# Kernel tuning notes

Hardware: AMD Instinct MI355X
Metric: run time of the kernel (lower is better)

Reference implementation:

```python
import jax, jax.numpy as jnp
import numpy as np

N_NODES = 100000
N_EDGE_PAIRS = 800000  # undirected pairs -> 1.6M directed edges
DIM_IN = 128
NUM_CLASSES = 16
N_ITERS = 5


def _log_normalize(a):
    return a - jax.nn.logsumexp(a, axis=-1, keepdims=True)


def setup_inputs() -> dict:
    key = jax.random.key(0)
    k1, k2, k3, k4, k5 = jax.random.split(key, 5)
    # reciprocal directed edges: edges 2i and 2i+1 are reverses of each other
    src = jax.random.randint(k1, (N_EDGE_PAIRS,), 0, N_NODES)
    dst = jax.random.randint(k2, (N_EDGE_PAIRS,), 0, N_NODES)
    e_src = jnp.stack([src, dst], axis=1).reshape(-1)  # [E]
    e_dst = jnp.stack([dst, src], axis=1).reshape(-1)  # [E]
    edge_index = jnp.stack([e_src, e_dst], axis=0)     # [2, E]
    E = e_src.shape[0]
    rv = jnp.arange(E).reshape(-1, 2)[:, ::-1].reshape(-1)  # reverse-edge permutation
    x = jax.random.normal(k3, (N_NODES, DIM_IN), dtype=jnp.float32)
    W = jax.random.normal(k4, (DIM_IN, NUM_CLASSES), dtype=jnp.float32) * 0.1
    b = jnp.zeros((NUM_CLASSES,), dtype=jnp.float32)
    dim_param = NUM_CLASSES * (NUM_CLASSES + 1) // 2
    param = jax.random.normal(k5, (dim_param,), dtype=jnp.float32) * 0.1
    return {"x": x, "W": W, "b": b, "param": param,
            "edge_index": edge_index, "rv": rv}


def reference(x, W, b, param, edge_index, rv):
    N = x.shape[0]
    C = W.shape[1]
    # MLP (num_hidden=0 -> single Linear) + LogSoftmax
    log_b0 = jax.nn.log_softmax(x @ W + b, axis=-1)  # [N, C]
    # coupling matrix logH (symmetric), detached since learn_coupling=False
    rid, cid = np.tril_indices(C)
    logT = jnp.zeros((C, C), dtype=x.dtype).at[rid, cid].set(
        jax.nn.log_sigmoid(param * 10.0))
    logH = logT + jnp.triu(logT.T, 1)
    logH = jax.lax.stop_gradient(logH)
    src, dst = edge_index[0], edge_index[1]
    E = src.shape[0]
    log_msg = jnp.full((E, C), -float(np.log(C)), dtype=x.dtype)
    log_b = log_b0
    for _ in range(N_ITERS):
        # message: gather beliefs at source, subtract reverse message
        t = log_b[src] - log_msg[rv]                                    # [E, C]
        raw = jax.nn.logsumexp(t[:, :, None] + logH[None, :, :], axis=1)  # [E, C]
        log_msg = _log_normalize(raw)
        # aggregate (scatter-add) into destination nodes, then update
        agg = jax.ops.segment_sum(log_msg, dst, num_segments=N)         # [N, C]
        log_b = _log_normalize(agg + log_b0)
    return log_b
```

## Files before the change

kernel.cpp:

```cpp
#include <hip/hip_runtime.h>
#include <hip/hip_fp16.h>
#include <math.h>

#define NN      100000
#define EE      1600000
#define NPAIRS  800000
#define DIN     128
#define CC      16
#define NITERS  5
#define PPT     4
#define NGRP    (NPAIRS / PPT)
#define NEGLOGC (-2.772588722239781f)
#define FPSCALE 1048576.0f
#define FPINV   (1.0f / 1048576.0f)

typedef float  f4 __attribute__((ext_vector_type(4)));
typedef int    i2 __attribute__((ext_vector_type(2)));
typedef unsigned long long ull;

__device__ __forceinline__ unsigned short f2h(float f) {
    return __half_as_ushort(__float2half(f));
}
__device__ __forceinline__ float h2f(unsigned short u) {
    return __half2float(__ushort_as_half(u));
}
__device__ __forceinline__ unsigned int pack_h(float lo, float hi) {
    return (unsigned int)f2h(lo) | ((unsigned int)f2h(hi) << 16);
}

__global__ __launch_bounds__(256) void k_setup(
    const float* __restrict__ x, const float* __restrict__ W,
    const float* __restrict__ b, const float* __restrict__ param,
    float* __restrict__ M, float* __restrict__ logb0,
    unsigned int* __restrict__ agg32)
{
    if (blockIdx.x == 0 && threadIdx.x < CC * (CC + 1) / 2) {
        int i = threadIdx.x;
        int r = 0;
        while ((r + 1) * (r + 2) / 2 <= i) ++r;
        int c = i - r * (r + 1) / 2;
        float z = param[i] * 10.0f;
        float s = 1.0f / (1.0f + __expf(-z));
        M[r * CC + c] = s;
        if (r != c) M[c * CC + r] = s;
    }

    int idx = blockIdx.x * 256 + threadIdx.x;
    agg32[idx] = 0u;

    int node = idx >> 4;
    int cls  = idx & 15;
    const f4* xr4 = (const f4*)(x + (long)node * DIN);
    float acc = b[cls];
#pragma unroll 8
    for (int k4 = 0; k4 < DIN / 4; ++k4) {
        f4 xv = __builtin_nontemporal_load(xr4 + k4);
        acc = fmaf(xv.x, W[(4 * k4 + 0) * CC + cls], acc);
        acc = fmaf(xv.y, W[(4 * k4 + 1) * CC + cls], acc);
        acc = fmaf(xv.z, W[(4 * k4 + 2) * CC + cls], acc);
        acc = fmaf(xv.w, W[(4 * k4 + 3) * CC + cls], acc);
    }
    float m = acc;
    for (int off = 8; off; off >>= 1) m = fmaxf(m, __shfl_xor(m, off, 16));
    float s = __expf(acc - m);
    for (int off = 8; off; off >>= 1) s += __shfl_xor(s, off, 16);
    logb0[idx] = acc - m - __logf(s);
}

template <bool RD_MSG, bool WR_MSG>
__global__ __launch_bounds__(256, 4) void k_edges_t(
    const i2* __restrict__ esrc2, const i2* __restrict__ edst2,
    const float* __restrict__ logb, const float* __restrict__ Mg,
    unsigned int* __restrict__ msg2, ull* __restrict__ agg8)
{
    __shared__ float sM[CC * CC];
    __shared__ float sE[PPT][16 * 40];
    sM[threadIdx.x] = Mg[threadIdx.x];
    __syncthreads();

    const int lane = threadIdx.x & 15;
    const int gl   = threadIdx.x >> 4;
    const int g    = blockIdx.x * 16 + gl;

    float Hrow[CC];
#pragma unroll
    for (int k = 0; k < CC; ++k) Hrow[k] = sM[k * CC + lane];

    i2 s01[PPT], d01[PPT];
    unsigned int mold[PPT];
#pragma unroll
    for (int r = 0; r < PPT; ++r) {
        int p = g + r * NGRP;
        s01[r] = __builtin_nontemporal_load(esrc2 + p);
        d01[r] = __builtin_nontemporal_load(edst2 + p);
        if (RD_MSG)
            mold[r] = __builtin_nontemporal_load(msg2 + (long)p * CC + lane);
    }

    float lb0[PPT], lb1[PPT];
#pragma unroll
    for (int r = 0; r < PPT; ++r) {
        lb0[r] = logb[(long)s01[r].x * CC + lane];
        lb1[r] = logb[(long)s01[r].y * CC + lane];
    }

#pragma unroll
    for (int r = 0; r < PPT; ++r) {
        float mo0, mo1;
        if (RD_MSG) {
            mo0 = h2f((unsigned short)(mold[r] & 0xffffu));
            mo1 = h2f((unsigned short)(mold[r] >> 16));
        } else {
            mo0 = NEGLOGC; mo1 = NEGLOGC;
        }
        float* eb = sE[r] + gl * 40;
        eb[lane]      = __expf(lb0[r] - mo1);
        eb[16 + lane] = __expf(lb1[r] - mo0);
    }

#pragma unroll
    for (int r = 0; r < PPT; ++r) {
        const float* eb = sE[r] + gl * 40;
        float S0 = 0.f, S1 = 0.f;
#pragma unroll
        for (int ch = 0; ch < 4; ++ch) {
            f4 e0 = *(const f4*)(eb + 4 * ch);
            f4 e1 = *(const f4*)(eb + 16 + 4 * ch);
            S0 = fmaf(e0.x, Hrow[4 * ch + 0], S0);
            S0 = fmaf(e0.y, Hrow[4 * ch + 1], S0);
            S0 = fmaf(e0.z, Hrow[4 * ch + 2], S0);
            S0 = fmaf(e0.w, Hrow[4 * ch + 3], S0);
            S1 = fmaf(e1.x, Hrow[4 * ch + 0], S1);
            S1 = fmaf(e1.y, Hrow[4 * ch + 1], S1);
            S1 = fmaf(e1.z, Hrow[4 * ch + 2], S1);
            S1 = fmaf(e1.w, Hrow[4 * ch + 3], S1);
        }

        float T0 = S0, T1 = S1;
        for (int off = 8; off; off >>= 1) {
            T0 += __shfl_xor(T0, off, 16);
            T1 += __shfl_xor(T1, off, 16);
        }
        float tv = (lane & 1) ? T1 : T0;
        float lt = __logf(tv);
        float lp = __shfl_xor(lt, 1, 16);
        float lT0 = (lane & 1) ? lp : lt;
        float lT1 = (lane & 1) ? lt : lp;
        float n0 = __logf(S0) - lT0;
        float n1 = __logf(S1) - lT1;

        if (WR_MSG) {
            int p = g + r * NGRP;
            __builtin_nontemporal_store(pack_h(n0, n1),
                                        msg2 + (long)p * CC + lane);
        }

        unsigned int q0 = (unsigned int)(fmaxf(-n0, 0.f) * FPSCALE + 0.5f);
        unsigned int q1 = (unsigned int)(fmaxf(-n1, 0.f) * FPSCALE + 0.5f);
        unsigned int p0 = __shfl_xor(q0, 1, 16);
        unsigned int p1 = __shfl_xor(q1, 1, 16);
        bool odd = lane & 1;
        ull  val  = odd ? ((ull)p1 | ((ull)q1 << 32))
                        : ((ull)q0 | ((ull)p0 << 32));
        int  node = odd ? d01[r].y : d01[r].x;
        atomicAdd(&agg8[(long)node * 8 + (lane >> 1)], val);
    }
}

__global__ __launch_bounds__(256) void k_update(
    const float* __restrict__ logb0, unsigned int* __restrict__ agg32,
    float* __restrict__ out)
{
    int idx = blockIdx.x * blockDim.x + threadIdx.x;
    unsigned int q = agg32[idx];
    agg32[idx] = 0u;
    float v = fmaf(-(float)q, FPINV, logb0[idx]);
    float m = v;
    for (int off = 8; off; off >>= 1) m = fmaxf(m, __shfl_xor(m, off, 16));
    float s = __expf(v - m);
    for (int off = 8; off; off >>= 1) s += __shfl_xor(s, off, 16);
    out[idx] = v - m - __logf(s);
}

extern "C" void kernel_launch(void* const* d_in, const int* in_sizes, int n_in,
                              void* d_out, int out_size, void* d_ws, size_t ws_size,
                              hipStream_t stream)
{
    const float* x     = (const float*)d_in[0];
    const float* W     = (const float*)d_in[1];
    const float* b     = (const float*)d_in[2];
    const float* param = (const float*)d_in[3];
    const int*   eidx  = (const int*)d_in[4];
    const i2*    esrc2 = (const i2*)eidx;
    const i2*    edst2 = (const i2*)(eidx + EE);

    float* ws    = (float*)d_ws;
    float* M     = ws;
    float* logb0 = M     + 256;
    float* logb  = logb0 + (long)NN * CC;
    unsigned int* agg32 = (unsigned int*)(logb + (long)NN * CC);
    ull*          agg8  = (ull*)agg32;
    unsigned int* msg2  = agg32 + (long)NN * CC;

    k_setup<<<NN * CC / 256, 256, 0, stream>>>(x, W, b, param, M, logb0, agg32);

    const float* curb = logb0;
    for (int it = 0; it < NITERS; ++it) {
        if (it == 0)
            k_edges_t<false, true><<<NGRP / 16, 256, 0, stream>>>(
                esrc2, edst2, curb, M, msg2, agg8);
        else if (it == NITERS - 1)
            k_edges_t<true, false><<<NGRP / 16, 256, 0, stream>>>(
                esrc2, edst2, curb, M, msg2, agg8);
        else
            k_edges_t<true, true><<<NGRP / 16, 256, 0, stream>>>(
                esrc2, edst2, curb, M, msg2, agg8);
        float* dst = (it == NITERS - 1) ? (float*)d_out : logb;
        k_update<<<NN * CC / 256, 256, 0, stream>>>(logb0, agg32, dst);
        curb = dst;
    }
}
```

Measured before the change: 582.3 us.

## Compute edge message products with bf16 MFMA instead of scalar FMAs

Rewrites the edge kernel so each wavefront processes blocks of 16 directed edges and computes exp(belief-msg) times the coupling matrix with a bf16 16x16 MFMA, replacing the shared-memory staging and per-lane FMA loops. It also changes the per-lane data layout, with vector loads of beliefs and old messages per quad and a transposed output mapping for message stores and atomics. The aim is to cut VALU and LDS work per edge, in exchange for bf16 rounding of the exponentiated inputs and coupling matrix. It also drops the occupancy hint from the launch bounds.

```diff
diff --git a/kernel.cpp b/kernel.cpp
--- a/kernel.cpp
+++ b/kernel.cpp
@@ -8,14 +8,25 @@
 #define DIN     128
 #define CC      16
 #define NITERS  5
-#define PPT     4
-#define NGRP    (NPAIRS / PPT)
+#define UU      4
+#define NBLKS   (NPAIRS / 8)
+#define GRID_E  (NBLKS / (UU * 4))
 #define NEGLOGC (-2.772588722239781f)
 #define FPSCALE 1048576.0f
 #define FPINV   (1.0f / 1048576.0f)
 
-typedef float  f4 __attribute__((ext_vector_type(4)));
-typedef int    i2 __attribute__((ext_vector_type(2)));
+#if __has_builtin(__builtin_amdgcn_mfma_f32_16x16x16bf16_1k)
+#define USE_1K 1
+#else
+#define USE_1K 0
+#endif
+
+typedef float f4  __attribute__((ext_vector_type(4)));
+typedef float v4f __attribute__((ext_vector_type(4)));
+typedef short v4s __attribute__((ext_vector_type(4)));
+typedef short v8s __attribute__((ext_vector_type(8)));
+typedef unsigned int u4v __attribute__((ext_vector_type(4)));
+typedef int  i4v __attribute__((ext_vector_type(4)));
 typedef unsigned long long ull;
 
 __device__ __forceinline__ unsigned short f2h(float f) {
@@ -26,6 +37,11 @@
 }
 __device__ __forceinline__ unsigned int pack_h(float lo, float hi) {
     return (unsigned int)f2h(lo) | ((unsigned int)f2h(hi) << 16);
+}
+__device__ __forceinline__ unsigned short f2bf(float f) {
+    unsigned int u = __float_as_uint(f);
+    unsigned int r = u + 0x7fffu + ((u >> 16) & 1u);
+    return (unsigned short)(r >> 16);
 }
 
 __global__ __launch_bounds__(256) void k_setup(
@@ -68,102 +84,120 @@
 }
 
 template <bool RD_MSG, bool WR_MSG>
-__global__ __launch_bounds__(256, 4) void k_edges_t(
-    const i2* __restrict__ esrc2, const i2* __restrict__ edst2,
+__global__ __launch_bounds__(256) void k_edges_m(
+    const int* __restrict__ esrc, const int* __restrict__ edst,
     const float* __restrict__ logb, const float* __restrict__ Mg,
     unsigned int* __restrict__ msg2, ull* __restrict__ agg8)
 {
-    __shared__ float sM[CC * CC];
-    __shared__ float sE[PPT][16 * 40];
-    sM[threadIdx.x] = Mg[threadIdx.x];
-    __syncthreads();
-
-    const int lane = threadIdx.x & 15;
-    const int gl   = threadIdx.x >> 4;
-    const int g    = blockIdx.x * 16 + gl;
-
-    float Hrow[CC];
-#pragma unroll
-    for (int k = 0; k < CC; ++k) Hrow[k] = sM[k * CC + lane];
-
-    i2 s01[PPT], d01[PPT];
-    unsigned int mold[PPT];
-#pragma unroll
-    for (int r = 0; r < PPT; ++r) {
-        int p = g + r * NGRP;
-        s01[r] = __builtin_nontemporal_load(esrc2 + p);
-        d01[r] = __builtin_nontemporal_load(edst2 + p);
-        if (RD_MSG)
-            mold[r] = __builtin_nontemporal_load(msg2 + (long)p * CC + lane);
-    }
-
-    float lb0[PPT], lb1[PPT];
-#pragma unroll
-    for (int r = 0; r < PPT; ++r) {
-        lb0[r] = logb[(long)s01[r].x * CC + lane];
-        lb1[r] = logb[(long)s01[r].y * CC + lane];
-    }
-
-#pragma unroll
-    for (int r = 0; r < PPT; ++r) {
-        float mo0, mo1;
+    const int lane = threadIdx.x & 63;
+    const int wid  = blockIdx.x * 4 + (threadIdx.x >> 6);
+    const int m    = lane & 15;
+    const int q    = lane >> 4;
+
+#if USE_1K
+    v4s bfrag;
+#pragma unroll
+    for (int j = 0; j < 4; ++j)
+        bfrag[j] = (short)f2bf(Mg[(4 * q + j) * CC + m]);
+#else
+    v8s bfrag = {0, 0, 0, 0, 0, 0, 0, 0};
+    if (q < 2) {
+#pragma unroll
+        for (int j = 0; j < 8; ++j)
+            bfrag[j] = (short)f2bf(Mg[(8 * q + j) * CC + m]);
+    }
+#endif
+
+#pragma unroll
+    for (int u = 0; u < UU; ++u) {
+        const int  blk = wid * UU + u;
+        const long eb  = (long)blk * 16;
+        const long pb  = (long)blk * 8;
+        const long p   = pb + (m >> 1);
+
+        int src = __builtin_nontemporal_load(esrc + eb + m);
+
+        v4f acc = {0.f, 0.f, 0.f, 0.f};
+        v4f D;
+#if USE_1K
+        f4 lb = *(const f4*)(logb + (long)src * CC + 4 * q);
+        float mo[4];
         if (RD_MSG) {
-            mo0 = h2f((unsigned short)(mold[r] & 0xffffu));
-            mo1 = h2f((unsigned short)(mold[r] >> 16));
+            u4v mw = __builtin_nontemporal_load(
+                (const u4v*)(msg2 + p * CC + 4 * q));
+#pragma unroll
+            for (int j = 0; j < 4; ++j)
+                mo[j] = (m & 1) ? h2f((unsigned short)(mw[j] & 0xffffu))
+                                : h2f((unsigned short)(mw[j] >> 16));
         } else {
-            mo0 = NEGLOGC; mo1 = NEGLOGC;
-        }
-        float* eb = sE[r] + gl * 40;
-        eb[lane]      = __expf(lb0[r] - mo1);
-        eb[16 + lane] = __expf(lb1[r] - mo0);
-    }
-
-#pragma unroll
-    for (int r = 0; r < PPT; ++r) {
-        const float* eb = sE[r] + gl * 40;
-        float S0 = 0.f, S1 = 0.f;
-#pragma unroll
-        for (int ch = 0; ch < 4; ++ch) {
-            f4 e0 = *(const f4*)(eb + 4 * ch);
-            f4 e1 = *(const f4*)(eb + 16 + 4 * ch);
-            S0 = fmaf(e0.x, Hrow[4 * ch + 0], S0);
-            S0 = fmaf(e0.y, Hrow[4 * ch + 1], S0);
-            S0 = fmaf(e0.z, Hrow[4 * ch + 2], S0);
-            S0 = fmaf(e0.w, Hrow[4 * ch + 3], S0);
-            S1 = fmaf(e1.x, Hrow[4 * ch + 0], S1);
-            S1 = fmaf(e1.y, Hrow[4 * ch + 1], S1);
-            S1 = fmaf(e1.z, Hrow[4 * ch + 2], S1);
-            S1 = fmaf(e1.w, Hrow[4 * ch + 3], S1);
-        }
-
-        float T0 = S0, T1 = S1;
-        for (int off = 8; off; off >>= 1) {
-            T0 += __shfl_xor(T0, off, 16);
-            T1 += __shfl_xor(T1, off, 16);
-        }
-        float tv = (lane & 1) ? T1 : T0;
-        float lt = __logf(tv);
-        float lp = __shfl_xor(lt, 1, 16);
-        float lT0 = (lane & 1) ? lp : lt;
-        float lT1 = (lane & 1) ? lt : lp;
-        float n0 = __logf(S0) - lT0;
-        float n1 = __logf(S1) - lT1;
+#pragma unroll
+            for (int j = 0; j < 4; ++j) mo[j] = NEGLOGC;
+        }
+        v4s a;
+#pragma unroll
+        for (int j = 0; j < 4; ++j)
+            a[j] = (short)f2bf(__expf(lb[j] - mo[j]));
+        D = __builtin_amdgcn_mfma_f32_16x16x16bf16_1k(a, bfrag, acc, 0, 0, 0);
+#else
+        v8s a = {0, 0, 0, 0, 0, 0, 0, 0};
+        if (q < 2) {
+            f4 lbA = *(const f4*)(logb + (long)src * CC + 8 * q);
+            f4 lbB = *(const f4*)(logb + (long)src * CC + 8 * q + 4);
+            float mo[8];
+            if (RD_MSG) {
+                u4v mwA = __builtin_nontemporal_load(
+                    (const u4v*)(msg2 + p * CC + 8 * q));
+                u4v mwB = __builtin_nontemporal_load(
+                    (const u4v*)(msg2 + p * CC + 8 * q + 4));
+#pragma unroll
+                for (int j = 0; j < 4; ++j) {
+                    mo[j]     = (m & 1) ? h2f((unsigned short)(mwA[j] & 0xffffu))
+                                        : h2f((unsigned short)(mwA[j] >> 16));
+                    mo[4 + j] = (m & 1) ? h2f((unsigned short)(mwB[j] & 0xffffu))
+                                        : h2f((unsigned short)(mwB[j] >> 16));
+                }
+            } else {
+#pragma unroll
+                for (int j = 0; j < 8; ++j) mo[j] = NEGLOGC;
+            }
+#pragma unroll
+            for (int j = 0; j < 4; ++j) {
+                a[j]     = (short)f2bf(__expf(lbA[j] - mo[j]));
+                a[4 + j] = (short)f2bf(__expf(lbB[j] - mo[4 + j]));
+            }
+        }
+        D = __builtin_amdgcn_mfma_f32_16x16x32_bf16(a, bfrag, acc, 0, 0, 0);
+#endif
+
+        v4f T = D;
+#pragma unroll
+        for (int off = 1; off < 16; off <<= 1) {
+#pragma unroll
+            for (int i = 0; i < 4; ++i) T[i] += __shfl_xor(T[i], off, 16);
+        }
+        float n0 = __logf(D[0]) - __logf(T[0]);
+        float n1 = __logf(D[1]) - __logf(T[1]);
+        float n2 = __logf(D[2]) - __logf(T[2]);
+        float n3 = __logf(D[3]) - __logf(T[3]);
 
         if (WR_MSG) {
-            int p = g + r * NGRP;
             __builtin_nontemporal_store(pack_h(n0, n1),
-                                        msg2 + (long)p * CC + lane);
-        }
-
-        unsigned int q0 = (unsigned int)(fmaxf(-n0, 0.f) * FPSCALE + 0.5f);
-        unsigned int q1 = (unsigned int)(fmaxf(-n1, 0.f) * FPSCALE + 0.5f);
-        unsigned int p0 = __shfl_xor(q0, 1, 16);
-        unsigned int p1 = __shfl_xor(q1, 1, 16);
-        bool odd = lane & 1;
-        ull  val  = odd ? ((ull)p1 | ((ull)q1 << 32))
-                        : ((ull)q0 | ((ull)p0 << 32));
-        int  node = odd ? d01[r].y : d01[r].x;
-        atomicAdd(&agg8[(long)node * 8 + (lane >> 1)], val);
+                                        msg2 + (pb + 2 * q) * CC + m);
+            __builtin_nontemporal_store(pack_h(n2, n3),
+                                        msg2 + (pb + 2 * q + 1) * CC + m);
+        }
+
+        i4v d4 = *(const i4v*)(edst + eb + 4 * q);
+        float nv[4] = {n0, n1, n2, n3};
+#pragma unroll
+        for (int i = 0; i < 4; ++i) {
+            unsigned int qv = (unsigned int)(fmaxf(-nv[i], 0.f) * FPSCALE + 0.5f);
+            unsigned int pv = __shfl_xor(qv, 1, 16);
+            if (!(m & 1)) {
+                ull val = (ull)qv | ((ull)pv << 32);
+                atomicAdd(&agg8[(long)d4[i] * 8 + (m >> 1)], val);
+            }
+        }
     }
 }
 
@@ -191,8 +225,8 @@
     const float* b     = (const float*)d_in[2];
     const float* param = (const float*)d_in[3];
     const int*   eidx  = (const int*)d_in[4];
-    const i2*    esrc2 = (const i2*)eidx;
-    const i2*    edst2 = (const i2*)(eidx + EE);
+    const int*   esrc  = eidx;
+    const int*   edst  = eidx + EE;
 
     float* ws    = (float*)d_ws;
     float* M     = ws;
@@ -207,14 +241,14 @@
     const float* curb = logb0;
     for (int it = 0; it < NITERS; ++it) {
         if (it == 0)
-            k_edges_t<false, true><<<NGRP / 16, 256, 0, stream>>>(
-                esrc2, edst2, curb, M, msg2, agg8);
+            k_edges_m<false, true><<<GRID_E, 256, 0, stream>>>(
+                esrc, edst, curb, M, msg2, agg8);
         else if (it == NITERS - 1)
-            k_edges_t<true, false><<<NGRP / 16, 256, 0, stream>>>(
-                esrc2, edst2, curb, M, msg2, agg8);
+            k_edges_m<true, false><<<GRID_E, 256, 0, stream>>>(
+                esrc, edst, curb, M, msg2, agg8);
         else
-            k_edges_t<true, true><<<NGRP / 16, 256, 0, stream>>>(
-                esrc2, edst2, curb, M, msg2, agg8);
+            k_edges_m<true, true><<<GRID_E, 256, 0, stream>>>(
+                esrc, edst, curb, M, msg2, agg8);
         float* dst = (it == NITERS - 1) ? (float*)d_out : logb;
         k_update<<<NN * CC / 256, 256, 0, stream>>>(logb0, agg32, dst);
         curb = dst;
```

Result: no change. 574.1 us (-1.4%).
